# Performance work log

Measured on AMD Instinct MI355X. Metric: run time of the kernel, lower is better.

The kernel has to match this reference:

```python
import jax, jax.numpy as jnp
import numpy as np

B, T, H, L = 32, 1024, 1024, 2

def setup_inputs() -> dict:
    key = jax.random.key(0)
    k = jax.random.split(key, 5)
    scale = 1.0 / np.sqrt(H)  # keep tanh out of saturation, matches nn.Linear init scale
    x = jax.random.normal(k[0], (B, T, H), dtype=jnp.float32)
    Wx = jax.random.normal(k[1], (L, H, H), dtype=jnp.float32) * scale
    Wh = jax.random.normal(k[2], (L, H, H), dtype=jnp.float32) * scale
    bx = jax.random.normal(k[3], (L, H), dtype=jnp.float32) * scale
    bh = jax.random.normal(k[4], (L, H), dtype=jnp.float32) * scale
    return {"x": x, "Wx": Wx, "Wh": Wh, "bx": bx, "bh": bh}

def _run_layer(layer_in, Wx_l, Wh_l, bx_l, bh_l):
    # layer_in: [B, T, H]. Precompute input projection for all timesteps at once,
    # then scan the sequential recurrence h_t = tanh(x_proj_t + h_{t-1} @ Wh^T + bh).
    x_proj = jnp.einsum('bti,hi->bth', layer_in, Wx_l) + bx_l  # [B, T, H]
    Wh_T = Wh_l.T

    def step(h, xp_t):
        h_new = jnp.tanh(xp_t + h @ Wh_T + bh_l)
        return h_new, h_new

    h0 = jnp.zeros((B, H), dtype=layer_in.dtype)
    h_last, outs = jax.lax.scan(step, h0, jnp.swapaxes(x_proj, 0, 1))  # outs: [T, B, H]
    return jnp.swapaxes(outs, 0, 1), h_last

def reference(x, Wx, Wh, bx, bh):
    layer_in = x
    h_finals = []
    for l in range(L):  # small fixed layer count
        layer_in, h_last = _run_layer(layer_in, Wx[l], Wh[l], bx[l], bh[l])
        h_finals.append(h_last)
    outputs = layer_in                 # [B, T, H]
    h_n = jnp.stack(h_finals, axis=0)  # [L, B, H]
    return outputs, h_n
```

## Files before the change

### kernel.cpp

```cpp
#include <hip/hip_runtime.h>

#define BB 32
#define TT 1024
#define HH 1024
#define R0 32
#define P0 32
#define P1 8
#define NP 16

typedef float f32x4 __attribute__((ext_vector_type(4)));
typedef short bf16x8 __attribute__((ext_vector_type(8)));
typedef unsigned uint4v __attribute__((ext_vector_type(4)));
typedef unsigned short u16;

__device__ __forceinline__ u16 f2bf(float f) {
  unsigned u = __builtin_bit_cast(unsigned, f);
  u += 0x7fffu + ((u >> 16) & 1u);
  return (u16)(u >> 16);
}
__device__ __forceinline__ float bf2f(u16 h) {
  return __builtin_bit_cast(float, (unsigned)h << 16);
}
__device__ __forceinline__ bf16x8 packhi(f32x4 a, f32x4 b) {
  bf16x8 r;
  r[0] = (short)f2bf(a[0]); r[1] = (short)f2bf(a[1]);
  r[2] = (short)f2bf(a[2]); r[3] = (short)f2bf(a[3]);
  r[4] = (short)f2bf(b[0]); r[5] = (short)f2bf(b[1]);
  r[6] = (short)f2bf(b[2]); r[7] = (short)f2bf(b[3]);
  return r;
}
__device__ __forceinline__ bf16x8 packlo(f32x4 a, f32x4 b, bf16x8 hi) {
  bf16x8 r;
  r[0] = (short)f2bf(a[0] - bf2f((u16)hi[0]));
  r[1] = (short)f2bf(a[1] - bf2f((u16)hi[1]));
  r[2] = (short)f2bf(a[2] - bf2f((u16)hi[2]));
  r[3] = (short)f2bf(a[3] - bf2f((u16)hi[3]));
  r[4] = (short)f2bf(b[0] - bf2f((u16)hi[4]));
  r[5] = (short)f2bf(b[1] - bf2f((u16)hi[5]));
  r[6] = (short)f2bf(b[2] - bf2f((u16)hi[6]));
  r[7] = (short)f2bf(b[3] - bf2f((u16)hi[7]));
  return r;
}
__device__ __forceinline__ bf16x8 mergelo(uint4v q0, uint4v q1) {
  uint4v r;
  r.x = __builtin_amdgcn_perm(q0.y, q0.x, 0x05040100u);
  r.y = __builtin_amdgcn_perm(q0.w, q0.z, 0x05040100u);
  r.z = __builtin_amdgcn_perm(q1.y, q1.x, 0x05040100u);
  r.w = __builtin_amdgcn_perm(q1.w, q1.z, 0x05040100u);
  return __builtin_bit_cast(bf16x8, r);
}
__device__ __forceinline__ bf16x8 mergehi(uint4v q0, uint4v q1) {
  uint4v r;
  r.x = __builtin_amdgcn_perm(q0.y, q0.x, 0x07060302u);
  r.y = __builtin_amdgcn_perm(q0.w, q0.z, 0x07060302u);
  r.z = __builtin_amdgcn_perm(q1.y, q1.x, 0x07060302u);
  r.w = __builtin_amdgcn_perm(q1.w, q1.z, 0x07060302u);
  return __builtin_bit_cast(bf16x8, r);
}
__device__ __forceinline__ void spin(const unsigned* p, unsigned tgt) {
  while (__hip_atomic_load(p, __ATOMIC_RELAXED, __HIP_MEMORY_SCOPE_AGENT) < tgt)
    __builtin_amdgcn_s_sleep(1);
}
#define MFMA __builtin_amdgcn_mfma_f32_16x16x32_bf16

__global__ __launch_bounds__(256, 1) void rnn_fused(
    const float* __restrict__ x, const float* __restrict__ Wx,
    const float* __restrict__ Wh, const float* __restrict__ bx,
    const float* __restrict__ bh, float* __restrict__ out,
    unsigned* __restrict__ ring0,
    unsigned* __restrict__ h1r,
    float* __restrict__ pj0,
    float* __restrict__ pj1,
    unsigned* __restrict__ flg)
{
  __shared__ float red[4][16 * 68];
  const int tid  = threadIdx.x;
  const int wg   = blockIdx.x;
  const int role  = wg >> 6;
  const int layer = (wg >> 5) & 1;
  const int bg    = (wg >> 4) & 1;
  const int idx   = wg & 15;
  const int n0    = idx << 6;
  const int b0    = bg << 4;
  const int lane  = tid & 63;
  const int wv    = tid >> 6;
  const int am    = lane & 15;
  const int aq    = lane >> 4;
  const int fragoff = (wv << 8) + (aq << 3);
  const int rowE = tid >> 4;
  const int cb   = tid & 15;

  const float* WM = (role == 0 ? Wh : Wx) + (size_t)layer * HH * HH;
  bf16x8 wHi[4][8], wLo[4][8];
  #pragma unroll
  for (int j = 0; j < 4; ++j) {
    const float* p = WM + (size_t)(n0 + (j << 4) + am) * HH + fragoff;
    #pragma unroll
    for (int ss = 0; ss < 8; ++ss) {
      f32x4 a = *(const f32x4*)(p + (ss << 5));
      f32x4 b = *(const f32x4*)(p + (ss << 5) + 4);
      wHi[j][ss] = packhi(a, b);
      wLo[j][ss] = packlo(a, b, wHi[j][ss]);
    }
  }
  const f32x4 z4 = {0.f, 0.f, 0.f, 0.f};

  if (role == 0) {
    const int gOwn = layer * 2 + bg;
    const int gPrj = 4 + layer * 2 + bg;
    const int gBP  = 6 + bg;
    for (int t = 0; t < TT; ++t) {
      const unsigned* pa = nullptr;
      if (lane < 4) {
        if (t >= 1) pa = flg + ((size_t)gOwn * TT + (t - 1)) * NP + (wv << 2) + lane;
      } else if (lane == 4) {
        pa = flg + ((size_t)gPrj * TT + t) * NP + idx;
      } else if (lane >= 8 && lane < 12 && layer == 0 && t >= R0) {
        pa = flg + ((size_t)gBP * TT + (t - R0)) * NP + (wv << 2) + (lane - 8);
      }
      if (pa) spin(pa, 1);
      __builtin_amdgcn_fence(__ATOMIC_ACQUIRE, "agent");

      const unsigned* hp = (layer == 0
            ? ring0 + (size_t)((t - 1) & (R0 - 1)) * (BB * HH)
            : h1r  + (size_t)((t - 1) & 1) * (BB * HH))
          + (b0 + am) * HH + fragoff;

      f32x4 accA[4] = {z4, z4, z4, z4};
      f32x4 accB[4] = {z4, z4, z4, z4};
      f32x4 accC[4] = {z4, z4, z4, z4};
      #pragma unroll
      for (int ss = 0; ss < 8; ++ss) {
        uint4v q0 = *(const uint4v*)(hp + (ss << 5));
        uint4v q1 = *(const uint4v*)(hp + (ss << 5) + 4);
        bf16x8 aH = mergelo(q0, q1);
        bf16x8 aL = mergehi(q0, q1);
        #pragma unroll
        for (int j = 0; j < 4; ++j) {
          accA[j] = MFMA(aH, wHi[j][ss], accA[j], 0, 0, 0);
          accB[j] = MFMA(aH, wLo[j][ss], accB[j], 0, 0, 0);
          accC[j] = MFMA(aL, wHi[j][ss], accC[j], 0, 0, 0);
        }
      }

      #pragma unroll
      for (int j = 0; j < 4; ++j) {
        f32x4 s = (accA[j] + accB[j]) + accC[j];
        #pragma unroll
        for (int i = 0; i < 4; ++i)
          red[wv][((aq << 2) + i) * 68 + (j << 4) + am] = s[i];
      }
      __syncthreads();

      const float* pjrow = (layer == 0
            ? pj0 + (size_t)(t & (P0 - 1)) * (BB * HH)
            : pj1 + (size_t)(t & (P1 - 1)) * (BB * HH))
          + (b0 + rowE) * HH + n0;
      unsigned* dst = (layer == 0
            ? ring0 + (size_t)(t & (R0 - 1)) * (BB * HH)
            : h1r  + (size_t)(t & 1) * (BB * HH))
          + (b0 + rowE) * HH + n0;

      float hv[4]; unsigned pk[4];
      #pragma unroll
      for (int k = 0; k < 4; ++k) {
        const int c = cb + (k << 4);
        float v = red[0][rowE * 68 + c] + red[1][rowE * 68 + c]
                + red[2][rowE * 68 + c] + red[3][rowE * 68 + c] + pjrow[c];
        hv[k] = tanhf(v);
        unsigned p0 = (unsigned)f2bf(hv[k]);
        p0 |= (unsigned)f2bf(hv[k] - bf2f((u16)p0)) << 16;
        pk[k] = p0;
      }
      #pragma unroll
      for (int k = 0; k < 4; ++k)
        __hip_atomic_store(&dst[cb + (k << 4)], pk[k],
                           __ATOMIC_RELAXED, __HIP_MEMORY_SCOPE_AGENT);
      __syncthreads();
      if (tid == 0)
        __hip_atomic_store(flg + ((size_t)gOwn * TT + t) * NP + idx, 1u,
                           __ATOMIC_RELEASE, __HIP_MEMORY_SCOPE_AGENT);

      if (layer == 1) {
        #pragma unroll
        for (int k = 0; k < 4; ++k)
          out[(size_t)(b0 + rowE) * (TT * HH) + (size_t)t * HH + n0 + cb + (k << 4)] = hv[k];
      }
      if (t == TT - 1) {
        #pragma unroll
        for (int k = 0; k < 4; ++k)
          out[(size_t)BB * TT * HH + (size_t)layer * (BB * HH)
              + (b0 + rowE) * HH + n0 + cb + (k << 4)] = hv[k];
      }
    }
  } else {
    const int gOut = 4 + layer * 2 + bg;
    const int gIn  = bg;
    const int gBPf = (layer == 0) ? bg : (2 + bg);
    const int Pd   = (layer == 0) ? P0 : P1;
    float* pring   = (layer == 0) ? pj0 : pj1;
    float bias[4];
    #pragma unroll
    for (int k = 0; k < 4; ++k)
      bias[k] = bx[layer * HH + n0 + cb + (k << 4)]
              + bh[layer * HH + n0 + cb + (k << 4)];

    for (int t = 0; t < TT; ++t) {
      const unsigned* pa = nullptr;
      if (lane < 4) {
        if (layer == 1) pa = flg + ((size_t)gIn * TT + t) * NP + (wv << 2) + lane;
      } else if (lane >= 8 && lane < 12 && t >= Pd) {
        pa = flg + ((size_t)gBPf * TT + (t - Pd)) * NP + (wv << 2) + (lane - 8);
      }
      if (pa) spin(pa, 1);
      if (layer == 1) __builtin_amdgcn_fence(__ATOMIC_ACQUIRE, "agent");

      f32x4 accA[4] = {z4, z4, z4, z4};
      f32x4 accB[4] = {z4, z4, z4, z4};
      f32x4 accC[4] = {z4, z4, z4, z4};
      if (layer == 0) {
        const float* xp = x + (size_t)(b0 + am) * (TT * HH) + (size_t)t * HH + fragoff;
        #pragma unroll
        for (int ss = 0; ss < 8; ++ss) {
          f32x4 a = *(const f32x4*)(xp + (ss << 5));
          f32x4 b = *(const f32x4*)(xp + (ss << 5) + 4);
          bf16x8 xh = packhi(a, b);
          bf16x8 xl = packlo(a, b, xh);
          #pragma unroll
          for (int j = 0; j < 4; ++j) {
            accA[j] = MFMA(xh, wHi[j][ss], accA[j], 0, 0, 0);
            accB[j] = MFMA(xh, wLo[j][ss], accB[j], 0, 0, 0);
            accC[j] = MFMA(xl, wHi[j][ss], accC[j], 0, 0, 0);
          }
        }
      } else {
        const unsigned* gp = ring0 + (size_t)(t & (R0 - 1)) * (BB * HH)
                           + (b0 + am) * HH + fragoff;
        #pragma unroll
        for (int ss = 0; ss < 8; ++ss) {
          uint4v q0 = *(const uint4v*)(gp + (ss << 5));
          uint4v q1 = *(const uint4v*)(gp + (ss << 5) + 4);
          bf16x8 gH = mergelo(q0, q1);
          bf16x8 gL = mergehi(q0, q1);
          #pragma unroll
          for (int j = 0; j < 4; ++j) {
            accA[j] = MFMA(gH, wHi[j][ss], accA[j], 0, 0, 0);
            accB[j] = MFMA(gH, wLo[j][ss], accB[j], 0, 0, 0);
            accC[j] = MFMA(gL, wHi[j][ss], accC[j], 0, 0, 0);
          }
        }
      }

      #pragma unroll
      for (int j = 0; j < 4; ++j) {
        f32x4 s = (accA[j] + accB[j]) + accC[j];
        #pragma unroll
        for (int i = 0; i < 4; ++i)
          red[wv][((aq << 2) + i) * 68 + (j << 4) + am] = s[i];
      }
      __syncthreads();

      float* dst = pring + (size_t)(t & (Pd - 1)) * (BB * HH)
                 + (b0 + rowE) * HH + n0;
      #pragma unroll
      for (int k = 0; k < 4; ++k) {
        const int c = cb + (k << 4);
        float v = red[0][rowE * 68 + c] + red[1][rowE * 68 + c]
                + red[2][rowE * 68 + c] + red[3][rowE * 68 + c] + bias[k];
        __hip_atomic_store(&dst[c], v, __ATOMIC_RELAXED, __HIP_MEMORY_SCOPE_AGENT);
      }
      __syncthreads();
      if (tid == 0)
        __hip_atomic_store(flg + ((size_t)gOut * TT + t) * NP + idx, 1u,
                           __ATOMIC_RELEASE, __HIP_MEMORY_SCOPE_AGENT);
    }
  }
}

__global__ void prep(unsigned* ring0, unsigned* h1r, unsigned* flg) {
  int i = blockIdx.x * 256 + threadIdx.x;
  if (i < BB * HH) {
    ring0[(size_t)(R0 - 1) * (BB * HH) + i] = 0;
    h1r[(size_t)(BB * HH) + i] = 0;
  }
  if (i < 8 * TT * NP) flg[i] = 0;
}

extern "C" void kernel_launch(void* const* d_in, const int* in_sizes, int n_in,
                              void* d_out, int out_size, void* d_ws, size_t ws_size,
                              hipStream_t stream) {
  const float* x  = (const float*)d_in[0];
  const float* Wx = (const float*)d_in[1];
  const float* Wh = (const float*)d_in[2];
  const float* bx = (const float*)d_in[3];
  const float* bh = (const float*)d_in[4];
  float* out = (float*)d_out;

  char* ws = (char*)d_ws;
  unsigned* ring0 = (unsigned*)ws;
  size_t o = (size_t)R0 * BB * HH * sizeof(unsigned);
  unsigned* h1r = (unsigned*)(ws + o);
  o += (size_t)2 * BB * HH * sizeof(unsigned);
  float* pj0 = (float*)(ws + o);
  o += (size_t)P0 * BB * HH * sizeof(float);
  float* pj1 = (float*)(ws + o);
  o += (size_t)P1 * BB * HH * sizeof(float);
  unsigned* flg = (unsigned*)(ws + o);

  prep<<<512, 256, 0, stream>>>(ring0, h1r, flg);
  rnn_fused<<<128, 256, 0, stream>>>(x, Wx, Wh, bx, bh, out,
                                     ring0, h1r, pj0, pj1, flg);
}
```

Baseline: 9.884 ms.

## Hoist layer-0 input projection into a separate GEMM and split recurrence per wave

The layer-0 input projection is moved out of the persistent pipelined kernel into a standalone bulk GEMM that writes x@Wx^T+bias into the output buffer as scratch. The recurrent kernel now gives each wave its own 16-column slice across the full K dimension, which removes the LDS cross-wave reduction and the __syncthreads from the serial critical path and gives per-wave flags. It drops to 96 persistent workgroups, with more weight registers held per wave. The intent is to shorten the per-timestep latency of the recurrence, at the cost of an extra pass over x and the output buffer before the recurrence starts.

```diff
diff --git a/kernel.cpp b/kernel.cpp
--- a/kernel.cpp
+++ b/kernel.cpp
@@ -3,10 +3,8 @@
 #define BB 32
 #define TT 1024
 #define HH 1024
-#define R0 32
-#define P0 32
-#define P1 8
-#define NP 16
+#define NR 32
+#define NP1 8
 
 typedef float f32x4 __attribute__((ext_vector_type(4)));
 typedef short bf16x8 __attribute__((ext_vector_type(8)));
@@ -63,25 +61,17 @@
 }
 #define MFMA __builtin_amdgcn_mfma_f32_16x16x32_bf16
 
-__global__ __launch_bounds__(256, 1) void rnn_fused(
+__global__ __launch_bounds__(256, 2) void xgemm(
     const float* __restrict__ x, const float* __restrict__ Wx,
-    const float* __restrict__ Wh, const float* __restrict__ bx,
-    const float* __restrict__ bh, float* __restrict__ out,
-    unsigned* __restrict__ ring0,
-    unsigned* __restrict__ h1r,
-    float* __restrict__ pj0,
-    float* __restrict__ pj1,
-    unsigned* __restrict__ flg)
+    const float* __restrict__ bx, const float* __restrict__ bh,
+    float* __restrict__ xp)
 {
   __shared__ float red[4][16 * 68];
-  const int tid  = threadIdx.x;
-  const int wg   = blockIdx.x;
-  const int role  = wg >> 6;
-  const int layer = (wg >> 5) & 1;
-  const int bg    = (wg >> 4) & 1;
-  const int idx   = wg & 15;
-  const int n0    = idx << 6;
-  const int b0    = bg << 4;
+  const int tid   = threadIdx.x;
+  const int strip = blockIdx.x & 15;
+  const int chunk = blockIdx.x >> 4;
+  const int n0    = strip << 6;
+  const int m0    = chunk << 10;
   const int lane  = tid & 63;
   const int wv    = tid >> 6;
   const int am    = lane & 15;
@@ -90,11 +80,10 @@
   const int rowE = tid >> 4;
   const int cb   = tid & 15;
 
-  const float* WM = (role == 0 ? Wh : Wx) + (size_t)layer * HH * HH;
   bf16x8 wHi[4][8], wLo[4][8];
   #pragma unroll
   for (int j = 0; j < 4; ++j) {
-    const float* p = WM + (size_t)(n0 + (j << 4) + am) * HH + fragoff;
+    const float* p = Wx + (size_t)(n0 + (j << 4) + am) * HH + fragoff;
     #pragma unroll
     for (int ss = 0; ss < 8; ++ss) {
       f32x4 a = *(const f32x4*)(p + (ss << 5));
@@ -103,175 +92,199 @@
       wLo[j][ss] = packlo(a, b, wHi[j][ss]);
     }
   }
+  float bias[4];
+  #pragma unroll
+  for (int k = 0; k < 4; ++k)
+    bias[k] = bx[n0 + cb + (k << 4)] + bh[n0 + cb + (k << 4)];
   const f32x4 z4 = {0.f, 0.f, 0.f, 0.f};
 
-  if (role == 0) {
-    const int gOwn = layer * 2 + bg;
-    const int gPrj = 4 + layer * 2 + bg;
-    const int gBP  = 6 + bg;
+  for (int it = 0; it < 64; ++it) {
+    const int r0 = m0 + (it << 4);
+    const float* xr = x + (size_t)(r0 + am) * HH + fragoff;
+    f32x4 accA[4] = {z4, z4, z4, z4};
+    f32x4 accB[4] = {z4, z4, z4, z4};
+    f32x4 accC[4] = {z4, z4, z4, z4};
+    #pragma unroll
+    for (int ss = 0; ss < 8; ++ss) {
+      f32x4 a = *(const f32x4*)(xr + (ss << 5));
+      f32x4 b = *(const f32x4*)(xr + (ss << 5) + 4);
+      bf16x8 xh = packhi(a, b);
+      bf16x8 xl = packlo(a, b, xh);
+      #pragma unroll
+      for (int j = 0; j < 4; ++j) {
+        accA[j] = MFMA(xh, wHi[j][ss], accA[j], 0, 0, 0);
+        accB[j] = MFMA(xh, wLo[j][ss], accB[j], 0, 0, 0);
+        accC[j] = MFMA(xl, wHi[j][ss], accC[j], 0, 0, 0);
+      }
+    }
+    #pragma unroll
+    for (int j = 0; j < 4; ++j) {
+      f32x4 s = (accA[j] + accB[j]) + accC[j];
+      #pragma unroll
+      for (int i = 0; i < 4; ++i)
+        red[wv][((aq << 2) + i) * 68 + (j << 4) + am] = s[i];
+    }
+    __syncthreads();
+    #pragma unroll
+    for (int k = 0; k < 4; ++k) {
+      const int c = cb + (k << 4);
+      float v = red[0][rowE * 68 + c] + red[1][rowE * 68 + c]
+              + red[2][rowE * 68 + c] + red[3][rowE * 68 + c] + bias[k];
+      xp[(size_t)(r0 + rowE) * HH + n0 + c] = v;
+    }
+    __syncthreads();
+  }
+}
+
+__global__ __launch_bounds__(256, 1) void rnn_pipe(
+    const float* __restrict__ Wx, const float* __restrict__ Wh,
+    const float* __restrict__ bx, const float* __restrict__ bh,
+    float* __restrict__ out,
+    unsigned* __restrict__ ring0,
+    unsigned* __restrict__ h1r,
+    float* __restrict__ pj1,
+    unsigned* __restrict__ flg)
+{
+  const int tid  = threadIdx.x;
+  const int wg   = blockIdx.x;
+  const int role = wg >> 5;
+  const int bg   = (wg >> 4) & 1;
+  const int idx  = wg & 15;
+  const int lane = tid & 63;
+  const int wv   = tid >> 6;
+  const int am   = lane & 15;
+  const int aq   = lane >> 4;
+  const int p    = (idx << 2) | wv;
+  const int wcb  = p << 4;
+  const int b0   = bg << 4;
+  const int row0 = aq << 2;
+
+  const float* WM = (role == 0) ? Wh
+                  : (role == 1) ? Wh + (size_t)HH * HH
+                                : Wx + (size_t)HH * HH;
+  bf16x8 wHi[32], wLo[32];
+  {
+    const float* wp = WM + (size_t)(wcb + am) * HH + (aq << 3);
+    #pragma unroll
+    for (int ss = 0; ss < 32; ++ss) {
+      f32x4 a = *(const f32x4*)(wp + (ss << 5));
+      f32x4 b = *(const f32x4*)(wp + (ss << 5) + 4);
+      wHi[ss] = packhi(a, b);
+      wLo[ss] = packlo(a, b, wHi[ss]);
+    }
+  }
+  const f32x4 z4 = {0.f, 0.f, 0.f, 0.f};
+
+  if (role < 2) {
+    const int gOwn = role * 2 + bg;
     for (int t = 0; t < TT; ++t) {
-      const unsigned* pa = nullptr;
-      if (lane < 4) {
-        if (t >= 1) pa = flg + ((size_t)gOwn * TT + (t - 1)) * NP + (wv << 2) + lane;
-      } else if (lane == 4) {
-        pa = flg + ((size_t)gPrj * TT + t) * NP + idx;
-      } else if (lane >= 8 && lane < 12 && layer == 0 && t >= R0) {
-        pa = flg + ((size_t)gBP * TT + (t - R0)) * NP + (wv << 2) + (lane - 8);
-      }
-      if (pa) spin(pa, 1);
+      if (t >= 1) spin(flg + (((size_t)gOwn * TT + (t - 1)) << 6) + lane, 1);
+      if (role == 0) {
+        if ((t & 7) == 0 && t >= NR)
+          spin(flg + (((size_t)(4 + bg) * TT + (t - 25)) << 6) + lane, 1);
+      } else {
+        if (lane == 0)
+          spin(flg + (((size_t)(4 + bg) * TT + t) << 6) + p, 1);
+      }
       __builtin_amdgcn_fence(__ATOMIC_ACQUIRE, "agent");
 
-      const unsigned* hp = (layer == 0
-            ? ring0 + (size_t)((t - 1) & (R0 - 1)) * (BB * HH)
+      float pjv[4];
+      if (role == 0) {
+        const float* q = out + ((size_t)(b0 + row0) * TT + t) * HH + wcb + am;
+        #pragma unroll
+        for (int i = 0; i < 4; ++i) pjv[i] = q[(size_t)i * TT * HH];
+      } else {
+        const float* q = pj1 + (size_t)(t & (NP1 - 1)) * (BB * HH)
+                       + (b0 + row0) * HH + wcb + am;
+        #pragma unroll
+        for (int i = 0; i < 4; ++i) pjv[i] = q[i * HH];
+      }
+
+      const unsigned* hp = (role == 0
+            ? ring0 + (size_t)((t - 1) & (NR - 1)) * (BB * HH)
             : h1r  + (size_t)((t - 1) & 1) * (BB * HH))
-          + (b0 + am) * HH + fragoff;
-
-      f32x4 accA[4] = {z4, z4, z4, z4};
-      f32x4 accB[4] = {z4, z4, z4, z4};
-      f32x4 accC[4] = {z4, z4, z4, z4};
-      #pragma unroll
-      for (int ss = 0; ss < 8; ++ss) {
+          + (b0 + am) * HH + (aq << 3);
+
+      f32x4 aA = z4, aB = z4, aC = z4;
+      #pragma unroll
+      for (int ss = 0; ss < 32; ++ss) {
         uint4v q0 = *(const uint4v*)(hp + (ss << 5));
         uint4v q1 = *(const uint4v*)(hp + (ss << 5) + 4);
         bf16x8 aH = mergelo(q0, q1);
         bf16x8 aL = mergehi(q0, q1);
-        #pragma unroll
-        for (int j = 0; j < 4; ++j) {
-          accA[j] = MFMA(aH, wHi[j][ss], accA[j], 0, 0, 0);
-          accB[j] = MFMA(aH, wLo[j][ss], accB[j], 0, 0, 0);
-          accC[j] = MFMA(aL, wHi[j][ss], accC[j], 0, 0, 0);
-        }
-      }
-
-      #pragma unroll
-      for (int j = 0; j < 4; ++j) {
-        f32x4 s = (accA[j] + accB[j]) + accC[j];
+        aA = MFMA(aH, wHi[ss], aA, 0, 0, 0);
+        aB = MFMA(aH, wLo[ss], aB, 0, 0, 0);
+        aC = MFMA(aL, wHi[ss], aC, 0, 0, 0);
+      }
+      f32x4 acc = (aA + aB) + aC;
+
+      float hv[4]; unsigned pk[4];
+      #pragma unroll
+      for (int i = 0; i < 4; ++i) {
+        float v = acc[i] + pjv[i];
+        hv[i] = tanhf(v);
+        unsigned pw = (unsigned)f2bf(hv[i]);
+        pw |= (unsigned)f2bf(hv[i] - bf2f((u16)pw)) << 16;
+        pk[i] = pw;
+      }
+      unsigned* dst = (role == 0
+            ? ring0 + (size_t)(t & (NR - 1)) * (BB * HH)
+            : h1r  + (size_t)(t & 1) * (BB * HH))
+          + (b0 + row0) * HH + wcb + am;
+      #pragma unroll
+      for (int i = 0; i < 4; ++i)
+        __hip_atomic_store(dst + i * HH, pk[i],
+                           __ATOMIC_RELAXED, __HIP_MEMORY_SCOPE_AGENT);
+      if (lane == 0)
+        __hip_atomic_store(flg + (((size_t)gOwn * TT + t) << 6) + p, 1u,
+                           __ATOMIC_RELEASE, __HIP_MEMORY_SCOPE_AGENT);
+
+      if (role == 1) {
+        float* ob = out + (size_t)(b0 + row0) * (TT * HH) + (size_t)t * HH + wcb + am;
         #pragma unroll
         for (int i = 0; i < 4; ++i)
-          red[wv][((aq << 2) + i) * 68 + (j << 4) + am] = s[i];
-      }
-      __syncthreads();
-
-      const float* pjrow = (layer == 0
-            ? pj0 + (size_t)(t & (P0 - 1)) * (BB * HH)
-            : pj1 + (size_t)(t & (P1 - 1)) * (BB * HH))
-          + (b0 + rowE) * HH + n0;
-      unsigned* dst = (layer == 0
-            ? ring0 + (size_t)(t & (R0 - 1)) * (BB * HH)
-            : h1r  + (size_t)(t & 1) * (BB * HH))
-          + (b0 + rowE) * HH + n0;
-
-      float hv[4]; unsigned pk[4];
-      #pragma unroll
-      for (int k = 0; k < 4; ++k) {
-        const int c = cb + (k << 4);
-        float v = red[0][rowE * 68 + c] + red[1][rowE * 68 + c]
-                + red[2][rowE * 68 + c] + red[3][rowE * 68 + c] + pjrow[c];
-        hv[k] = tanhf(v);
-        unsigned p0 = (unsigned)f2bf(hv[k]);
-        p0 |= (unsigned)f2bf(hv[k] - bf2f((u16)p0)) << 16;
-        pk[k] = p0;
-      }
-      #pragma unroll
-      for (int k = 0; k < 4; ++k)
-        __hip_atomic_store(&dst[cb + (k << 4)], pk[k],
-                           __ATOMIC_RELAXED, __HIP_MEMORY_SCOPE_AGENT);
-      __syncthreads();
-      if (tid == 0)
-        __hip_atomic_store(flg + ((size_t)gOwn * TT + t) * NP + idx, 1u,
-                           __ATOMIC_RELEASE, __HIP_MEMORY_SCOPE_AGENT);
-
-      if (layer == 1) {
-        #pragma unroll
-        for (int k = 0; k < 4; ++k)
-          out[(size_t)(b0 + rowE) * (TT * HH) + (size_t)t * HH + n0 + cb + (k << 4)] = hv[k];
+          __builtin_nontemporal_store(hv[i], ob + (size_t)i * TT * HH);
       }
       if (t == TT - 1) {
-        #pragma unroll
-        for (int k = 0; k < 4; ++k)
-          out[(size_t)BB * TT * HH + (size_t)layer * (BB * HH)
-              + (b0 + rowE) * HH + n0 + cb + (k << 4)] = hv[k];
-      }
-    }
-  } else {
-    const int gOut = 4 + layer * 2 + bg;
-    const int gIn  = bg;
-    const int gBPf = (layer == 0) ? bg : (2 + bg);
-    const int Pd   = (layer == 0) ? P0 : P1;
-    float* pring   = (layer == 0) ? pj0 : pj1;
-    float bias[4];
-    #pragma unroll
-    for (int k = 0; k < 4; ++k)
-      bias[k] = bx[layer * HH + n0 + cb + (k << 4)]
-              + bh[layer * HH + n0 + cb + (k << 4)];
-
-    for (int t = 0; t < TT; ++t) {
-      const unsigned* pa = nullptr;
-      if (lane < 4) {
-        if (layer == 1) pa = flg + ((size_t)gIn * TT + t) * NP + (wv << 2) + lane;
-      } else if (lane >= 8 && lane < 12 && t >= Pd) {
-        pa = flg + ((size_t)gBPf * TT + (t - Pd)) * NP + (wv << 2) + (lane - 8);
-      }
-      if (pa) spin(pa, 1);
-      if (layer == 1) __builtin_amdgcn_fence(__ATOMIC_ACQUIRE, "agent");
-
-      f32x4 accA[4] = {z4, z4, z4, z4};
-      f32x4 accB[4] = {z4, z4, z4, z4};
-      f32x4 accC[4] = {z4, z4, z4, z4};
-      if (layer == 0) {
-        const float* xp = x + (size_t)(b0 + am) * (TT * HH) + (size_t)t * HH + fragoff;
-        #pragma unroll
-        for (int ss = 0; ss < 8; ++ss) {
-          f32x4 a = *(const f32x4*)(xp + (ss << 5));
-          f32x4 b = *(const f32x4*)(xp + (ss << 5) + 4);
-          bf16x8 xh = packhi(a, b);
-          bf16x8 xl = packlo(a, b, xh);
-          #pragma unroll
-          for (int j = 0; j < 4; ++j) {
-            accA[j] = MFMA(xh, wHi[j][ss], accA[j], 0, 0, 0);
-            accB[j] = MFMA(xh, wLo[j][ss], accB[j], 0, 0, 0);
-            accC[j] = MFMA(xl, wHi[j][ss], accC[j], 0, 0, 0);
-          }
-        }
-      } else {
-        const unsigned* gp = ring0 + (size_t)(t & (R0 - 1)) * (BB * HH)
-                           + (b0 + am) * HH + fragoff;
-        #pragma unroll
-        for (int ss = 0; ss < 8; ++ss) {
-          uint4v q0 = *(const uint4v*)(gp + (ss << 5));
-          uint4v q1 = *(const uint4v*)(gp + (ss << 5) + 4);
-          bf16x8 gH = mergelo(q0, q1);
-          bf16x8 gL = mergehi(q0, q1);
-          #pragma unroll
-          for (int j = 0; j < 4; ++j) {
-            accA[j] = MFMA(gH, wHi[j][ss], accA[j], 0, 0, 0);
-            accB[j] = MFMA(gH, wLo[j][ss], accB[j], 0, 0, 0);
-            accC[j] = MFMA(gL, wHi[j][ss], accC[j], 0, 0, 0);
-          }
-        }
-      }
-
-      #pragma unroll
-      for (int j = 0; j < 4; ++j) {
-        f32x4 s = (accA[j] + accB[j]) + accC[j];
+        float* hb = out + (size_t)BB * TT * HH + (size_t)role * (BB * HH)
+                  + (b0 + row0) * HH + wcb + am;
         #pragma unroll
         for (int i = 0; i < 4; ++i)
-          red[wv][((aq << 2) + i) * 68 + (j << 4) + am] = s[i];
-      }
-      __syncthreads();
-
-      float* dst = pring + (size_t)(t & (Pd - 1)) * (BB * HH)
-                 + (b0 + rowE) * HH + n0;
-      #pragma unroll
-      for (int k = 0; k < 4; ++k) {
-        const int c = cb + (k << 4);
-        float v = red[0][rowE * 68 + c] + red[1][rowE * 68 + c]
-                + red[2][rowE * 68 + c] + red[3][rowE * 68 + c] + bias[k];
-        __hip_atomic_store(&dst[c], v, __ATOMIC_RELAXED, __HIP_MEMORY_SCOPE_AGENT);
-      }
-      __syncthreads();
-      if (tid == 0)
-        __hip_atomic_store(flg + ((size_t)gOut * TT + t) * NP + idx, 1u,
+          __builtin_nontemporal_store(hv[i], hb + i * HH);
+      }
+    }
+  } else {
+    const float biasv = bx[HH + wcb + am] + bh[HH + wcb + am];
+    for (int t = 0; t < TT; ++t) {
+      spin(flg + (((size_t)bg * TT + t) << 6) + lane, 1);
+      if ((t & 3) == 0 && t >= NP1)
+        spin(flg + (((size_t)(2 + bg) * TT + (t - 5)) << 6) + lane, 1);
+      __builtin_amdgcn_fence(__ATOMIC_ACQUIRE, "agent");
+
+      const unsigned* hp = ring0 + (size_t)(t & (NR - 1)) * (BB * HH)
+                         + (b0 + am) * HH + (aq << 3);
+      f32x4 aA = z4, aB = z4, aC = z4;
+      #pragma unroll
+      for (int ss = 0; ss < 32; ++ss) {
+        uint4v q0 = *(const uint4v*)(hp + (ss << 5));
+        uint4v q1 = *(const uint4v*)(hp + (ss << 5) + 4);
+        bf16x8 aH = mergelo(q0, q1);
+        bf16x8 aL = mergehi(q0, q1);
+        aA = MFMA(aH, wHi[ss], aA, 0, 0, 0);
+        aB = MFMA(aH, wLo[ss], aB, 0, 0, 0);
+        aC = MFMA(aL, wHi[ss], aC, 0, 0, 0);
+      }
+      f32x4 acc = (aA + aB) + aC;
+
+      float* dst = pj1 + (size_t)(t & (NP1 - 1)) * (BB * HH)
+                 + (b0 + row0) * HH + wcb + am;
+      #pragma unroll
+      for (int i = 0; i < 4; ++i)
+        __hip_atomic_store((unsigned*)(dst + i * HH),
+                           __builtin_bit_cast(unsigned, acc[i] + biasv),
+                           __ATOMIC_RELAXED, __HIP_MEMORY_SCOPE_AGENT);
+      if (lane == 0)
+        __hip_atomic_store(flg + (((size_t)(4 + bg) * TT + t) << 6) + p, 1u,
                            __ATOMIC_RELEASE, __HIP_MEMORY_SCOPE_AGENT);
     }
   }
@@ -280,10 +293,10 @@
 __global__ void prep(unsigned* ring0, unsigned* h1r, unsigned* flg) {
   int i = blockIdx.x * 256 + threadIdx.x;
   if (i < BB * HH) {
-    ring0[(size_t)(R0 - 1) * (BB * HH) + i] = 0;
+    ring0[(size_t)(NR - 1) * (BB * HH) + i] = 0;
     h1r[(size_t)(BB * HH) + i] = 0;
   }
-  if (i < 8 * TT * NP) flg[i] = 0;
+  if (i < 6 * TT * 64) flg[i] = 0;
 }
 
 extern "C" void kernel_launch(void* const* d_in, const int* in_sizes, int n_in,
@@ -298,16 +311,15 @@
 
   char* ws = (char*)d_ws;
   unsigned* ring0 = (unsigned*)ws;
-  size_t o = (size_t)R0 * BB * HH * sizeof(unsigned);
+  size_t o = (size_t)NR * BB * HH * sizeof(unsigned);
   unsigned* h1r = (unsigned*)(ws + o);
   o += (size_t)2 * BB * HH * sizeof(unsigned);
-  float* pj0 = (float*)(ws + o);
-  o += (size_t)P0 * BB * HH * sizeof(float);
   float* pj1 = (float*)(ws + o);
-  o += (size_t)P1 * BB * HH * sizeof(float);
+  o += (size_t)NP1 * BB * HH * sizeof(float);
   unsigned* flg = (unsigned*)(ws + o);
 
-  prep<<<512, 256, 0, stream>>>(ring0, h1r, flg);
-  rnn_fused<<<128, 256, 0, stream>>>(x, Wx, Wh, bx, bh, out,
-                                     ring0, h1r, pj0, pj1, flg);
-}
+  prep<<<1536, 256, 0, stream>>>(ring0, h1r, flg);
+  xgemm<<<512, 256, 0, stream>>>(x, Wx, bx, bh, out);
+  rnn_pipe<<<96, 256, 0, stream>>>(Wx, Wh, bx, bh, out,
+                                   ring0, h1r, pj1, flg);
+}
```

Result: slower. 24.59 ms (+148.7%).
